# Performance work log

Hardware: AMD Instinct MI355X
Metric: run time of the kernel (lower is better)

Reference implementation:

```python
import jax, jax.numpy as jnp
import numpy as np

D_MODEL = 1024
N_DIM = 64      # per-head dim; scores scaled by 1/sqrt(n_dim)
N_HEADS = 16
SEQ = 4096
LN_EPS = 1e-5


def setup_inputs() -> dict:
    key = jax.random.key(0)
    ks = jax.random.split(key, 12)
    hd = N_HEADS * N_DIM  # == D_MODEL (required by residual add)
    s = 0.02
    return {
        "embed_word_vec": jax.random.normal(ks[0], (SEQ, D_MODEL), dtype=jnp.float32),
        "attn_mask": jax.random.uniform(ks[1], (SEQ, SEQ)) < 0.1,  # True = masked out
        "wq": jax.random.normal(ks[2], (D_MODEL, hd), dtype=jnp.float32) * s,
        "bq": jnp.zeros((hd,), dtype=jnp.float32),
        "wk": jax.random.normal(ks[3], (D_MODEL, hd), dtype=jnp.float32) * s,
        "bk": jnp.zeros((hd,), dtype=jnp.float32),
        "wv": jax.random.normal(ks[4], (D_MODEL, hd), dtype=jnp.float32) * s,
        "bv": jnp.zeros((hd,), dtype=jnp.float32),
        "wo": jax.random.normal(ks[5], (hd, D_MODEL), dtype=jnp.float32) * s,
        "bo": jnp.zeros((D_MODEL,), dtype=jnp.float32),
        "gamma": jnp.ones((D_MODEL,), dtype=jnp.float32),
        "beta": jnp.zeros((D_MODEL,), dtype=jnp.float32),
    }


def reference(embed_word_vec, attn_mask, wq, bq, wk, bk, wv, bv, wo, bo, gamma, beta):
    x = embed_word_vec                      # [S, d_model]
    q = x @ wq + bq                         # [S, H*D]
    k = x @ wk + bk
    v = x @ wv + bv
    scores = (q @ k.T) / jnp.sqrt(jnp.asarray(N_DIM, dtype=q.dtype))  # [S, S]
    scores = jnp.where(attn_mask, jnp.asarray(-jnp.inf, dtype=scores.dtype), scores)
    attention = jax.nn.softmax(scores, axis=-1)                       # [S, S]
    context = attention @ v + x             # AV + residual, [S, d_model]
    h = context @ wo + bo                   # out projection
    # LayerNorm over last dim
    mu = jnp.mean(h, axis=-1, keepdims=True)
    var = jnp.mean(jnp.square(h - mu), axis=-1, keepdims=True)
    output = (h - mu) * jax.lax.rsqrt(var + LN_EPS) * gamma + beta
    return (output, attention)
```

## Files before the change

### kernel.cpp

```cpp
#include <hip/hip_runtime.h>
#include <hip/hip_bf16.h>
#include <stdint.h>

#define SEQ 4096
#define DM  1024

typedef __attribute__((ext_vector_type(8))) short bf16x8;
typedef __attribute__((ext_vector_type(4))) float f32x4;

template <int V> struct Int { static constexpr int v = V; };

__device__ __forceinline__ short f2bf(float f) {
  union { float f; unsigned int i; } x; x.f = f;
  unsigned int r = x.i + 0x7FFFu + ((x.i >> 16) & 1u);
  return (short)(r >> 16);
}
__device__ __forceinline__ float bf2f(short s) {
  union { unsigned int i; float f; } u;
  u.i = ((unsigned int)(unsigned short)s) << 16;
  return u.f;
}

__device__ __forceinline__ void gload16(const short* g, short* l) {
  __builtin_amdgcn_global_load_lds(
      (const __attribute__((address_space(1))) unsigned int*)g,
      (__attribute__((address_space(3))) unsigned int*)l, 16, 0, 0);
}

__device__ __forceinline__ float wave_max(float v) {
#pragma unroll
  for (int o = 32; o; o >>= 1) v = fmaxf(v, __shfl_xor(v, o));
  return v;
}
__device__ __forceinline__ float wave_sum(float v) {
#pragma unroll
  for (int o = 32; o; o >>= 1) v += __shfl_xor(v, o);
  return v;
}

#define BARRIER() do { asm volatile("" ::: "memory"); \
  __builtin_amdgcn_s_barrier(); asm volatile("" ::: "memory"); } while (0)
#define MF(a, b, c) __builtin_amdgcn_mfma_f32_16x16x32_bf16(a, b, c, 0, 0, 0)

template <int EPI>
__global__ __launch_bounds__(512, 2) void gemm8(
    const short* __restrict__ A, const short* __restrict__ B,
    short* __restrict__ C, short* __restrict__ Cv,
    const float* __restrict__ bias, int Ksplit, int lda, int ldb, int ldc,
    int ldv, float scale, int ntm, int ntn, long csplit, int pc) {
  __shared__ short lds[2][4][8192];
  const int tid = threadIdx.x;
  const int lane = tid & 63;
  const int wid = tid >> 6;
  const int wr = wid >> 2;
  const int wc = wid & 3;
  const int bid = blockIdx.x, nwg = gridDim.x;
  const int chunk = nwg >> 3;
  const int wl = (bid & 7) * chunk + (bid >> 3);
  const int tpg = ntm * ntn;
  const int split = wl / tpg;
  const int r0 = wl - split * tpg;
  const int q = r0 / chunk, i0 = r0 % chunk;
  const int npatch = ntn / pc;
  const int m0 = ((q / npatch) * (chunk / pc) + i0 / pc) * 256;
  const int n0 = ((q % npatch) * pc + i0 % pc) * 256;
  const short* Ab = A + (long)split * Ksplit;
  const short* Bb = B + (long)split * Ksplit;
  short* Co = C + (long)split * csplit;

  const int o0 = tid * 16;
  const int oo = o0 ^ (((o0 >> 7) & 7) << 4);
  const int sr0 = oo >> 7;
  const int sc0 = (oo & 127) >> 1;

  auto stA = [&](int buf, int h, int kt) {
    const short* g = Ab + (long)(m0 + h * 128 + sr0) * lda + kt * 64 + sc0;
    short* l = &lds[buf][h][0] + wid * 512;
    gload16(g, l);
    gload16(g + (long)64 * lda, l + 4096);
  };
  auto stB = [&](int buf, int h, int kt) {
    const short* g = Bb + (long)(n0 + h * 128 + sr0) * ldb + kt * 64 + sc0;
    short* l = &lds[buf][2 + h][0] + wid * 512;
    gload16(g, l);
    gload16(g + (long)64 * ldb, l + 4096);
  };

  const int ll = lane & 15, lh = lane >> 4;
  auto ldaf = [&](int buf, int c, int mm, int kk) {
    const int r = c * 32 + mm * 16 + ll;
    const int off = (r * 64 + kk * 32 + lh * 8) ^ ((r & 7) << 3);
    return *(const bf16x8*)(&lds[buf][wr][0] + off);
  };
  auto ldbf = [&](int buf, int n, int kk) {
    const int r = (wc & 1) * 64 + n * 16 + ll;
    const int off = (r * 64 + kk * 32 + lh * 8) ^ ((r & 7) << 3);
    return *(const bf16x8*)(&lds[buf][2 + (wc >> 1)][0] + off);
  };

  f32x4 acc[8][4];
#pragma unroll
  for (int i = 0; i < 8; i++)
#pragma unroll
    for (int j = 0; j < 4; j++) acc[i][j] = (f32x4){0.f, 0.f, 0.f, 0.f};
  bf16x8 Bf[4][2];

  const int NT = Ksplit >> 6;
  stB(0, 0, 0); stB(0, 1, 0);
  stA(0, 0, 0); stA(0, 1, 0);
  stB(1, 0, 1); stB(1, 1, 1);
  asm volatile("s_waitcnt vmcnt(4)" ::: "memory");
  BARRIER();

  auto phase = [&](auto BUF, auto CC, auto LB, auto BARv, auto&& stg) {
    constexpr int buf = decltype(BUF)::v;
    constexpr int c = decltype(CC)::v;
    if constexpr (decltype(LB)::v != 0) {
#pragma unroll
      for (int n = 0; n < 4; n++) {
        Bf[n][0] = ldbf(buf, n, 0);
        Bf[n][1] = ldbf(buf, n, 1);
      }
    }
    bf16x8 a00 = ldaf(buf, c, 0, 0), a01 = ldaf(buf, c, 0, 1);
    bf16x8 a10 = ldaf(buf, c, 1, 0), a11 = ldaf(buf, c, 1, 1);
    stg();
    if constexpr (decltype(BARv)::v != 0) BARRIER();
    __builtin_amdgcn_s_setprio(1);
#pragma unroll
    for (int n = 0; n < 4; n++) {
      acc[2 * c][n] = MF(a00, Bf[n][0], acc[2 * c][n]);
      acc[2 * c][n] = MF(a01, Bf[n][1], acc[2 * c][n]);
      acc[2 * c + 1][n] = MF(a10, Bf[n][0], acc[2 * c + 1][n]);
      acc[2 * c + 1][n] = MF(a11, Bf[n][1], acc[2 * c + 1][n]);
    }
    __builtin_amdgcn_s_setprio(0);
  };

  for (int t = 0; t < NT; t += 2) {
    const bool nl = (t + 2 < NT);
    phase(Int<0>{}, Int<0>{}, Int<1>{}, Int<0>{},
          [&] { stA(1, 0, t + 1); stA(1, 1, t + 1); });
    phase(Int<0>{}, Int<1>{}, Int<0>{}, Int<1>{}, [] {});
    phase(Int<0>{}, Int<2>{}, Int<0>{}, Int<0>{},
          [&] { if (nl) { stB(0, 0, t + 2); stB(0, 1, t + 2); } });
    phase(Int<0>{}, Int<3>{}, Int<0>{}, Int<0>{}, [] {});
    if (nl) { asm volatile("s_waitcnt vmcnt(4)" ::: "memory"); }
    else    { asm volatile("s_waitcnt vmcnt(0)" ::: "memory"); }
    BARRIER();
    phase(Int<1>{}, Int<0>{}, Int<1>{}, Int<0>{},
          [&] { if (nl) { stA(0, 0, t + 2); stA(0, 1, t + 2); } });
    phase(Int<1>{}, Int<1>{}, Int<0>{}, Int<1>{}, [] {});
    phase(Int<1>{}, Int<2>{}, Int<0>{}, Int<0>{},
          [&] { if (nl) { stB(1, 0, t + 3); stB(1, 1, t + 3); } });
    phase(Int<1>{}, Int<3>{}, Int<0>{}, Int<0>{}, [] {});
    if (nl) {
      asm volatile("s_waitcnt vmcnt(4)" ::: "memory");
      BARRIER();
    }
  }

  const int rb = m0 + wr * 128 + lh * 4;
  const int cb0 = n0 + wc * 64 + ll;
  if (EPI == 3 && n0 >= 2048) {
#pragma unroll
    for (int mi = 0; mi < 8; mi++) {
#pragma unroll
      for (int n = 0; n < 4; n++) {
        const int col = cb0 + n * 16;
        const float bv = bias[col];
        short4 pk;
        pk.x = f2bf(acc[mi][n][0] + bv);
        pk.y = f2bf(acc[mi][n][1] + bv);
        pk.z = f2bf(acc[mi][n][2] + bv);
        pk.w = f2bf(acc[mi][n][3] + bv);
        *(short4*)(Cv + (long)(col - 2048) * ldv + rb + mi * 16) = pk;
      }
    }
    return;
  }
#pragma unroll
  for (int mi = 0; mi < 8; mi++) {
#pragma unroll
    for (int n = 0; n < 4; n++) {
      const int col = cb0 + n * 16;
      float bv = 0.f;
      if (EPI == 1 || EPI == 3) bv = bias[col];
#pragma unroll
      for (int r = 0; r < 4; r++) {
        const int row = rb + mi * 16 + r;
        const long off = (long)row * ldc + col;
        float v = acc[mi][n][r];
        if (EPI == 1 || EPI == 3) v += bv;
        if (EPI == 2) v *= scale;
        Co[off] = f2bf(v);
      }
    }
  }
}


__global__ __launch_bounds__(256) void cvt_f32_to_bf16(
    const float* __restrict__ in, short* __restrict__ out, int n4) {
  int i = blockIdx.x * 256 + threadIdx.x;
  if (i < n4) {
    float4 f = ((const float4*)in)[i];
    short4 o;
    o.x = f2bf(f.x); o.y = f2bf(f.y); o.z = f2bf(f.z); o.w = f2bf(f.w);
    ((short4*)out)[i] = o;
  }
}

__global__ void transpose_w4(const float* __restrict__ s0,
                             const float* __restrict__ s1,
                             const float* __restrict__ s2,
                             const float* __restrict__ s3,
                             short* __restrict__ d0, short* __restrict__ d1,
                             short* __restrict__ d2, short* __restrict__ d3) {
  const int z = blockIdx.z;
  const float* in = z == 0 ? s0 : z == 1 ? s1 : z == 2 ? s2 : s3;
  short* out = z == 0 ? d0 : z == 1 ? d1 : z == 2 ? d2 : d3;
  __shared__ float tile[32][33];
  const int bx = blockIdx.x * 32;
  const int by = blockIdx.y * 32;
  const int tx = threadIdx.x, ty = threadIdx.y;
#pragma unroll
  for (int i = 0; i < 32; i += 8)
    tile[ty + i][tx] = in[(long)(by + ty + i) * 1024 + bx + tx];
  __syncthreads();
#pragma unroll
  for (int i = 0; i < 32; i += 8)
    out[(long)(bx + ty + i) * 1024 + by + tx] = f2bf(tile[tx][ty + i]);
}

__global__ __launch_bounds__(256) void concat_bias(
    const float* __restrict__ bq, const float* __restrict__ bk,
    const float* __restrict__ bv, float* __restrict__ o) {
  int i = blockIdx.x * 256 + threadIdx.x;
  float v = (i < 1024) ? bq[i] : (i < 2048 ? bk[i - 1024] : bv[i - 2048]);
  o[i] = v;
}

template <int FUSED>
__global__ __launch_bounds__(256) void softmax_rows(const short* __restrict__ Sb,
                                                    const int* __restrict__ mask,
                                                    short* __restrict__ Pb,
                                                    float* __restrict__ Af,
                                                    int ld) {
  const long row = blockIdx.x;
  const bf16x8* src = (const bf16x8*)(Sb + row * ld);
  const int* mrow = mask + row * (long)SEQ;
  bf16x8* dst = (bf16x8*)(Pb + row * SEQ);
  const int tid = threadIdx.x;
  const int wid = tid >> 6, lane = tid & 63;
  bf16x8 a = src[tid], b = src[tid + 256];
  int4 ma0 = *(const int4*)(mrow + tid * 8);
  int4 ma1 = *(const int4*)(mrow + tid * 8 + 4);
  int4 mb0 = *(const int4*)(mrow + 2048 + tid * 8);
  int4 mb1 = *(const int4*)(mrow + 2048 + tid * 8 + 4);
  float v[16];
#pragma unroll
  for (int j = 0; j < 8; j++) { v[j] = bf2f(a[j]); v[8 + j] = bf2f(b[j]); }
  const int* mm0 = (const int*)&ma0;
  const int* mm1 = (const int*)&ma1;
  const int* mm2 = (const int*)&mb0;
  const int* mm3 = (const int*)&mb1;
#pragma unroll
  for (int j = 0; j < 4; j++) {
    if (mm0[j]) v[j] = -INFINITY;
    if (mm1[j]) v[4 + j] = -INFINITY;
    if (mm2[j]) v[8 + j] = -INFINITY;
    if (mm3[j]) v[12 + j] = -INFINITY;
  }
  float mx = -INFINITY;
#pragma unroll
  for (int j = 0; j < 16; j++) mx = fmaxf(mx, v[j]);
  mx = wave_max(mx);
  __shared__ float red[4];
  if (lane == 0) red[wid] = mx;
  __syncthreads();
  mx = fmaxf(fmaxf(red[0], red[1]), fmaxf(red[2], red[3]));
  float sum = 0.f;
#pragma unroll
  for (int j = 0; j < 16; j++) {
    v[j] = __expf(v[j] - mx);
    sum += v[j];
  }
  sum = wave_sum(sum);
  __shared__ float red2[4];
  if (lane == 0) red2[wid] = sum;
  __syncthreads();
  sum = red2[0] + red2[1] + red2[2] + red2[3];
  const float inv = 1.0f / sum;
  bf16x8 o0, o1;
#pragma unroll
  for (int j = 0; j < 8; j++) {
    v[j] *= inv;
    v[8 + j] *= inv;
    o0[j] = f2bf(v[j]);
    o1[j] = f2bf(v[8 + j]);
  }
  dst[tid] = o0;
  dst[tid + 256] = o1;
  if (FUSED) {
    float* orow = Af + row * (long)SEQ;
    *(float4*)(orow + tid * 8) = (float4){v[0], v[1], v[2], v[3]};
    *(float4*)(orow + tid * 8 + 4) = (float4){v[4], v[5], v[6], v[7]};
    *(float4*)(orow + 2048 + tid * 8) = (float4){v[8], v[9], v[10], v[11]};
    *(float4*)(orow + 2048 + tid * 8 + 4) = (float4){v[12], v[13], v[14], v[15]};
  }
}

__global__ __launch_bounds__(256) void expand_bf16_f32(
    const short* __restrict__ in, float* __restrict__ out) {
  long i = (long)blockIdx.x * 256 + threadIdx.x;
  bf16x8 a = ((const bf16x8*)in)[i];
  float4 lo, hi;
  lo.x = bf2f(a[0]); lo.y = bf2f(a[1]); lo.z = bf2f(a[2]); lo.w = bf2f(a[3]);
  hi.x = bf2f(a[4]); hi.y = bf2f(a[5]); hi.z = bf2f(a[6]); hi.w = bf2f(a[7]);
  ((float4*)out)[2 * i] = lo;
  ((float4*)out)[2 * i + 1] = hi;
}

__global__ __launch_bounds__(256) void reduce_ctx4(
    const short* __restrict__ p, const float* __restrict__ x,
    short* __restrict__ cb) {
  const long i = (long)blockIdx.x * 256 + threadIdx.x;
  bf16x8 a = ((const bf16x8*)p)[i];
  bf16x8 b = ((const bf16x8*)(p + 4194304))[i];
  bf16x8 c = ((const bf16x8*)(p + 8388608))[i];
  bf16x8 d = ((const bf16x8*)(p + 12582912))[i];
  float4 x0 = ((const float4*)x)[2 * i];
  float4 x1 = ((const float4*)x)[2 * i + 1];
  float xs[8] = {x0.x, x0.y, x0.z, x0.w, x1.x, x1.y, x1.z, x1.w};
  bf16x8 o;
#pragma unroll
  for (int j = 0; j < 8; j++)
    o[j] = f2bf(bf2f(a[j]) + bf2f(b[j]) + bf2f(c[j]) + bf2f(d[j]) + xs[j]);
  ((bf16x8*)cb)[i] = o;
}

__global__ __launch_bounds__(256) void ln4(
    const short* __restrict__ ph, const float* __restrict__ bo,
    const float* __restrict__ gamma, const float* __restrict__ beta,
    float* __restrict__ out) {
  const long row = blockIdx.x;
  const int tid = threadIdx.x;
  const int wid = tid >> 6, lane = tid & 63;
  const long base = row * DM + tid * 4;
  short4 p0 = *(const short4*)(ph + base);
  short4 p1 = *(const short4*)(ph + 4194304 + base);
  short4 p2 = *(const short4*)(ph + 8388608 + base);
  short4 p3 = *(const short4*)(ph + 12582912 + base);
  float4 bb = *(const float4*)(bo + tid * 4);
  float v[4];
  v[0] = bf2f(p0.x) + bf2f(p1.x) + bf2f(p2.x) + bf2f(p3.x) + bb.x;
  v[1] = bf2f(p0.y) + bf2f(p1.y) + bf2f(p2.y) + bf2f(p3.y) + bb.y;
  v[2] = bf2f(p0.z) + bf2f(p1.z) + bf2f(p2.z) + bf2f(p3.z) + bb.z;
  v[3] = bf2f(p0.w) + bf2f(p1.w) + bf2f(p2.w) + bf2f(p3.w) + bb.w;
  float s = v[0] + v[1] + v[2] + v[3];
  s = wave_sum(s);
  __shared__ float red[4];
  if (lane == 0) red[wid] = s;
  __syncthreads();
  const float mu = (red[0] + red[1] + red[2] + red[3]) * (1.f / DM);
  float var = 0.f;
#pragma unroll
  for (int j = 0; j < 4; j++) {
    float d = v[j] - mu;
    var += d * d;
  }
  var = wave_sum(var);
  __shared__ float red2[4];
  if (lane == 0) red2[wid] = var;
  __syncthreads();
  var = (red2[0] + red2[1] + red2[2] + red2[3]) * (1.f / DM);
  const float inv = rsqrtf(var + 1e-5f);
  float4 g = *(const float4*)(gamma + tid * 4);
  float4 be = *(const float4*)(beta + tid * 4);
  float4 o;
  o.x = (v[0] - mu) * inv * g.x + be.x;
  o.y = (v[1] - mu) * inv * g.y + be.y;
  o.z = (v[2] - mu) * inv * g.z + be.z;
  o.w = (v[3] - mu) * inv * g.w + be.w;
  *(float4*)(out + base) = o;
}

extern "C" void kernel_launch(void* const* d_in, const int* in_sizes, int n_in,
                              void* d_out, int out_size, void* d_ws,
                              size_t ws_size, hipStream_t stream) {
  const float* x    = (const float*)d_in[0];
  const int* mask   = (const int*)d_in[1];
  const float* wq   = (const float*)d_in[2];
  const float* bq   = (const float*)d_in[3];
  const float* wk   = (const float*)d_in[4];
  const float* bk   = (const float*)d_in[5];
  const float* wv   = (const float*)d_in[6];
  const float* bv   = (const float*)d_in[7];
  const float* wo   = (const float*)d_in[8];
  const float* bo   = (const float*)d_in[9];
  const float* gamma = (const float*)d_in[10];
  const float* beta  = (const float*)d_in[11];

  float* out  = (float*)d_out;
  float* attn = out + 4194304;
  short* cbuf = (short*)out;

  char* w = (char*)d_ws;
  const bool fused = ws_size >= (size_t)83886080 + 16384;
  short* Sb   = fused ? (short*)attn + 4096 : (short*)attn;
  const int ldS = fused ? 8192 : 4096;
  short* pav  = fused ? (short*)(w + 50331648) : (short*)attn;
  short* phh  = fused ? pav : (short*)(attn + 8388608);
  float* bqkv = fused ? (float*)(w + 83886080) : (float*)(w + 50331648);

  short* wqkvT = (short*)(w + 0);
  short* woT   = (short*)(w + 6291456);
  short* xb    = (short*)(w + 8388608);
  short* qkv   = (short*)(w + 16777216);
  short* attnb = (short*)(w + 8388608);
  short* vT    = (short*)(w + 41943040);

  cvt_f32_to_bf16<<<4096, 256, 0, stream>>>(x, xb, 1048576);
  transpose_w4<<<dim3(32, 32, 4), dim3(32, 8), 0, stream>>>(
      wq, wk, wv, wo, wqkvT, wqkvT + 1048576, wqkvT + 2097152, woT);
  concat_bias<<<12, 256, 0, stream>>>(bq, bk, bv, bqkv);

  gemm8<3><<<192, 512, 0, stream>>>(xb, wqkvT, qkv, vT, bqkv,
                                    1024, 1024, 1024, 3072, 4096, 1.f,
                                    16, 12, 0, 6);

  gemm8<2><<<256, 512, 0, stream>>>(qkv, qkv + 1024, Sb, nullptr, nullptr,
                                    1024, 3072, 3072, ldS, 0, 0.125f,
                                    16, 16, 0, 8);

  if (fused)
    softmax_rows<1><<<SEQ, 256, 0, stream>>>(Sb, mask, attnb, attn, ldS);
  else
    softmax_rows<0><<<SEQ, 256, 0, stream>>>(Sb, mask, attnb, attn, ldS);

  gemm8<0><<<256, 512, 0, stream>>>(attnb, vT, pav, nullptr, nullptr,
                                    1024, 4096, 4096, 1024, 0, 1.f,
                                    16, 4, 4194304L, 4);

  reduce_ctx4<<<2048, 256, 0, stream>>>(pav, x, cbuf);

  gemm8<0><<<256, 512, 0, stream>>>(cbuf, woT, phh, nullptr, nullptr,
                                    256, 1024, 1024, 1024, 0, 1.f,
                                    16, 4, 4194304L, 4);

  ln4<<<SEQ, 256, 0, stream>>>(phh, bo, gamma, beta, out);

  if (!fused) expand_bf16_f32<<<8192, 256, 0, stream>>>(attnb, attn);
}
```

Before: 195.5 us.

## Split GEMM phases per k-half and merge prep kernels into one launch

The GEMM main loop now runs sixteen half-size phases instead of eight. Each phase loads only one k-half of the B and A fragments and issues half the MFMAs, with global-to-LDS stages interleaved more finely. This is meant to spread LDS reads and global loads more evenly across MFMA work and lower register pressure. Separately, the bf16 conversion of x, the weight transposes and the bias concatenation are merged into one kernel launch, removing two launches at the cost of extra per-block branching.

```diff
diff --git a/kernel.cpp b/kernel.cpp
--- a/kernel.cpp
+++ b/kernel.cpp
@@ -112,48 +112,57 @@
   asm volatile("s_waitcnt vmcnt(4)" ::: "memory");
   BARRIER();
 
-  auto phase = [&](auto BUF, auto CC, auto LB, auto BARv, auto&& stg) {
+  auto phase = [&](auto BUF, auto CC, auto KK, auto LBF, auto BARv,
+                   auto&& stg) {
     constexpr int buf = decltype(BUF)::v;
     constexpr int c = decltype(CC)::v;
-    if constexpr (decltype(LB)::v != 0) {
-#pragma unroll
-      for (int n = 0; n < 4; n++) {
-        Bf[n][0] = ldbf(buf, n, 0);
-        Bf[n][1] = ldbf(buf, n, 1);
-      }
-    }
-    bf16x8 a00 = ldaf(buf, c, 0, 0), a01 = ldaf(buf, c, 0, 1);
-    bf16x8 a10 = ldaf(buf, c, 1, 0), a11 = ldaf(buf, c, 1, 1);
+    constexpr int kk = decltype(KK)::v;
+    if constexpr (decltype(LBF)::v != 0) {
+#pragma unroll
+      for (int n = 0; n < 4; n++) Bf[n][kk] = ldbf(buf, n, kk);
+    }
+    bf16x8 a0 = ldaf(buf, c, 0, kk);
+    bf16x8 a1 = ldaf(buf, c, 1, kk);
     stg();
     if constexpr (decltype(BARv)::v != 0) BARRIER();
     __builtin_amdgcn_s_setprio(1);
 #pragma unroll
     for (int n = 0; n < 4; n++) {
-      acc[2 * c][n] = MF(a00, Bf[n][0], acc[2 * c][n]);
-      acc[2 * c][n] = MF(a01, Bf[n][1], acc[2 * c][n]);
-      acc[2 * c + 1][n] = MF(a10, Bf[n][0], acc[2 * c + 1][n]);
-      acc[2 * c + 1][n] = MF(a11, Bf[n][1], acc[2 * c + 1][n]);
+      acc[2 * c][n] = MF(a0, Bf[n][kk], acc[2 * c][n]);
+      acc[2 * c + 1][n] = MF(a1, Bf[n][kk], acc[2 * c + 1][n]);
     }
     __builtin_amdgcn_s_setprio(0);
   };
 
   for (int t = 0; t < NT; t += 2) {
     const bool nl = (t + 2 < NT);
-    phase(Int<0>{}, Int<0>{}, Int<1>{}, Int<0>{},
-          [&] { stA(1, 0, t + 1); stA(1, 1, t + 1); });
-    phase(Int<0>{}, Int<1>{}, Int<0>{}, Int<1>{}, [] {});
-    phase(Int<0>{}, Int<2>{}, Int<0>{}, Int<0>{},
-          [&] { if (nl) { stB(0, 0, t + 2); stB(0, 1, t + 2); } });
-    phase(Int<0>{}, Int<3>{}, Int<0>{}, Int<0>{}, [] {});
+    phase(Int<0>{}, Int<0>{}, Int<0>{}, Int<1>{}, Int<0>{},
+          [&] { stA(1, 0, t + 1); });
+    phase(Int<0>{}, Int<0>{}, Int<1>{}, Int<1>{}, Int<1>{},
+          [&] { stA(1, 1, t + 1); });
+    phase(Int<0>{}, Int<1>{}, Int<0>{}, Int<0>{}, Int<0>{},
+          [&] { if (nl) stB(0, 0, t + 2); });
+    phase(Int<0>{}, Int<1>{}, Int<1>{}, Int<0>{}, Int<0>{},
+          [&] { if (nl) stB(0, 1, t + 2); });
+    phase(Int<0>{}, Int<2>{}, Int<0>{}, Int<0>{}, Int<0>{}, [] {});
+    phase(Int<0>{}, Int<2>{}, Int<1>{}, Int<0>{}, Int<0>{}, [] {});
+    phase(Int<0>{}, Int<3>{}, Int<0>{}, Int<0>{}, Int<0>{}, [] {});
+    phase(Int<0>{}, Int<3>{}, Int<1>{}, Int<0>{}, Int<0>{}, [] {});
     if (nl) { asm volatile("s_waitcnt vmcnt(4)" ::: "memory"); }
     else    { asm volatile("s_waitcnt vmcnt(0)" ::: "memory"); }
     BARRIER();
-    phase(Int<1>{}, Int<0>{}, Int<1>{}, Int<0>{},
-          [&] { if (nl) { stA(0, 0, t + 2); stA(0, 1, t + 2); } });
-    phase(Int<1>{}, Int<1>{}, Int<0>{}, Int<1>{}, [] {});
-    phase(Int<1>{}, Int<2>{}, Int<0>{}, Int<0>{},
-          [&] { if (nl) { stB(1, 0, t + 3); stB(1, 1, t + 3); } });
-    phase(Int<1>{}, Int<3>{}, Int<0>{}, Int<0>{}, [] {});
+    phase(Int<1>{}, Int<0>{}, Int<0>{}, Int<1>{}, Int<0>{},
+          [&] { if (nl) stA(0, 0, t + 2); });
+    phase(Int<1>{}, Int<0>{}, Int<1>{}, Int<1>{}, Int<1>{},
+          [&] { if (nl) stA(0, 1, t + 2); });
+    phase(Int<1>{}, Int<1>{}, Int<0>{}, Int<0>{}, Int<0>{},
+          [&] { if (nl) stB(1, 0, t + 3); });
+    phase(Int<1>{}, Int<1>{}, Int<1>{}, Int<0>{}, Int<0>{},
+          [&] { if (nl) stB(1, 1, t + 3); });
+    phase(Int<1>{}, Int<2>{}, Int<0>{}, Int<0>{}, Int<0>{}, [] {});
+    phase(Int<1>{}, Int<2>{}, Int<1>{}, Int<0>{}, Int<0>{}, [] {});
+    phase(Int<1>{}, Int<3>{}, Int<0>{}, Int<0>{}, Int<0>{}, [] {});
+    phase(Int<1>{}, Int<3>{}, Int<1>{}, Int<0>{}, Int<0>{}, [] {});
     if (nl) {
       asm volatile("s_waitcnt vmcnt(4)" ::: "memory");
       BARRIER();
@@ -200,30 +209,42 @@
 }
 
 
-__global__ __launch_bounds__(256) void cvt_f32_to_bf16(
-    const float* __restrict__ in, short* __restrict__ out, int n4) {
-  int i = blockIdx.x * 256 + threadIdx.x;
-  if (i < n4) {
-    float4 f = ((const float4*)in)[i];
-    short4 o;
-    o.x = f2bf(f.x); o.y = f2bf(f.y); o.z = f2bf(f.z); o.w = f2bf(f.w);
-    ((short4*)out)[i] = o;
-  }
-}
-
-__global__ void transpose_w4(const float* __restrict__ s0,
-                             const float* __restrict__ s1,
-                             const float* __restrict__ s2,
-                             const float* __restrict__ s3,
-                             short* __restrict__ d0, short* __restrict__ d1,
-                             short* __restrict__ d2, short* __restrict__ d3) {
+__global__ void prep_all(const float* __restrict__ x, short* __restrict__ xb,
+                         const float* __restrict__ s0,
+                         const float* __restrict__ s1,
+                         const float* __restrict__ s2,
+                         const float* __restrict__ s3,
+                         short* __restrict__ d0, short* __restrict__ d1,
+                         short* __restrict__ d2, short* __restrict__ d3,
+                         const float* __restrict__ bq,
+                         const float* __restrict__ bk,
+                         const float* __restrict__ bv,
+                         float* __restrict__ bqkv) {
   const int z = blockIdx.z;
+  const int tx = threadIdx.x, ty = threadIdx.y;
+  if (z == 4) {
+    const int flat = (blockIdx.y * 32 + blockIdx.x) * 256 + ty * 32 + tx;
+    const float4* xs = (const float4*)x;
+    short4* xd = (short4*)xb;
+#pragma unroll
+    for (int j = 0; j < 4; j++) {
+      float4 f = xs[j * 262144 + flat];
+      short4 o;
+      o.x = f2bf(f.x); o.y = f2bf(f.y); o.z = f2bf(f.z); o.w = f2bf(f.w);
+      xd[j * 262144 + flat] = o;
+    }
+    if (flat < 3072) {
+      float v = (flat < 1024) ? bq[flat]
+                              : (flat < 2048 ? bk[flat - 1024] : bv[flat - 2048]);
+      bqkv[flat] = v;
+    }
+    return;
+  }
   const float* in = z == 0 ? s0 : z == 1 ? s1 : z == 2 ? s2 : s3;
   short* out = z == 0 ? d0 : z == 1 ? d1 : z == 2 ? d2 : d3;
   __shared__ float tile[32][33];
   const int bx = blockIdx.x * 32;
   const int by = blockIdx.y * 32;
-  const int tx = threadIdx.x, ty = threadIdx.y;
 #pragma unroll
   for (int i = 0; i < 32; i += 8)
     tile[ty + i][tx] = in[(long)(by + ty + i) * 1024 + bx + tx];
@@ -231,14 +252,6 @@
 #pragma unroll
   for (int i = 0; i < 32; i += 8)
     out[(long)(bx + ty + i) * 1024 + by + tx] = f2bf(tile[tx][ty + i]);
-}
-
-__global__ __launch_bounds__(256) void concat_bias(
-    const float* __restrict__ bq, const float* __restrict__ bk,
-    const float* __restrict__ bv, float* __restrict__ o) {
-  int i = blockIdx.x * 256 + threadIdx.x;
-  float v = (i < 1024) ? bq[i] : (i < 2048 ? bk[i - 1024] : bv[i - 2048]);
-  o[i] = v;
 }
 
 template <int FUSED>
@@ -421,10 +434,9 @@
   short* attnb = (short*)(w + 8388608);
   short* vT    = (short*)(w + 41943040);
 
-  cvt_f32_to_bf16<<<4096, 256, 0, stream>>>(x, xb, 1048576);
-  transpose_w4<<<dim3(32, 32, 4), dim3(32, 8), 0, stream>>>(
-      wq, wk, wv, wo, wqkvT, wqkvT + 1048576, wqkvT + 2097152, woT);
-  concat_bias<<<12, 256, 0, stream>>>(bq, bk, bv, bqkv);
+  prep_all<<<dim3(32, 32, 5), dim3(32, 8), 0, stream>>>(
+      x, xb, wq, wk, wv, wo, wqkvT, wqkvT + 1048576, wqkvT + 2097152, woT,
+      bq, bk, bv, bqkv);
 
   gemm8<3><<<192, 512, 0, stream>>>(xb, wqkvT, qkv, vT, bqkv,
                                     1024, 1024, 1024, 3072, 4096, 1.f,
```

Measured after the change: 190.8 us, median of 3. -2.4%, faster.
